# Performance work log

Hardware: AMD Instinct MI355X
Metric: run time of the kernel (lower is better)

The kernel has to match this reference:

```python
import jax, jax.numpy as jnp
import numpy as np

B, N, H, HEADS, F, L = 32, 256, 512, 8, 2048, 8
D = H // HEADS  # per-head dim
EPS = 1e-5


def _layernorm(x, scale, bias):
    mu = jnp.mean(x, axis=-1, keepdims=True)
    var = jnp.mean(jnp.square(x - mu), axis=-1, keepdims=True)
    return (x - mu) * jax.lax.rsqrt(var + EPS) * scale + bias


def setup_inputs() -> dict:
    key = jax.random.key(0)
    ks = jax.random.split(key, 12)
    s = 0.02
    inp = {
        "x": jax.random.normal(ks[0], (B, N, H), jnp.float32),
        "attn_bias": jax.random.normal(ks[1], (B, HEADS, N, N), jnp.float32),
        "ln1_s": jnp.ones((L, H), jnp.float32),
        "ln1_b": jnp.zeros((L, H), jnp.float32),
        "wq": s * jax.random.normal(ks[2], (L, H, H), jnp.float32),
        "bq": jnp.zeros((L, H), jnp.float32),
        "wk": s * jax.random.normal(ks[3], (L, H, H), jnp.float32),
        "bk": jnp.zeros((L, H), jnp.float32),
        "wv": s * jax.random.normal(ks[4], (L, H, H), jnp.float32),
        "bv": jnp.zeros((L, H), jnp.float32),
        "wo": s * jax.random.normal(ks[5], (L, H, H), jnp.float32),
        "bo": jnp.zeros((L, H), jnp.float32),
        "ln2_s": jnp.ones((L, H), jnp.float32),
        "ln2_b": jnp.zeros((L, H), jnp.float32),
        "w1": s * jax.random.normal(ks[6], (L, H, F), jnp.float32),
        "b1": jnp.zeros((L, F), jnp.float32),
        "w2": s * jax.random.normal(ks[7], (L, F, H), jnp.float32),
        "b2": jnp.zeros((L, H), jnp.float32),
    }
    return inp


def reference(x, attn_bias, ln1_s, ln1_b, wq, bq, wk, bk, wv, bv, wo, bo,
              ln2_s, ln2_b, w1, b1, w2, b2):
    scale = D ** (-0.5)
    for l in range(L):
        # --- self attention block ---
        y = _layernorm(x, ln1_s[l], ln1_b[l])
        q = (y @ wq[l] + bq[l]).reshape(B, N, HEADS, D) * scale
        k = (y @ wk[l] + bk[l]).reshape(B, N, HEADS, D)
        v = (y @ wv[l] + bv[l]).reshape(B, N, HEADS, D)
        scores = jnp.einsum("bqhd,bkhd->bhqk", q, k) + attn_bias
        probs = jax.nn.softmax(scores, axis=-1)
        ctx = jnp.einsum("bhqk,bkhd->bqhd", probs, v).reshape(B, N, H)
        x = x + ctx @ wo[l] + bo[l]
        # --- FFN block ---
        y = _layernorm(x, ln2_s[l], ln2_b[l])
        y = jax.nn.gelu(y @ w1[l] + b1[l], approximate=False)
        x = x + y @ w2[l] + b2[l]
    return x
```

## Files before the change

### kernel.cpp

```cpp
#include <hip/hip_runtime.h>
#include <hip/hip_bf16.h>
#include <math.h>

typedef __bf16 bf16;
typedef __bf16 bf16x8 __attribute__((ext_vector_type(8)));
typedef __bf16 bf16x4 __attribute__((ext_vector_type(4)));
typedef float  f32x4  __attribute__((ext_vector_type(4)));

#define DEV __device__ __forceinline__

DEV f32x4 mfma16(bf16x8 a, bf16x8 b, f32x4 c) {
    return __builtin_amdgcn_mfma_f32_16x16x32_bf16(a, b, c, 0, 0, 0);
}

DEV void gload16(const bf16* g, bf16* l) {
    __builtin_amdgcn_global_load_lds(
        (const __attribute__((address_space(1))) void*)g,
        (__attribute__((address_space(3))) void*)l, 16, 0, 0);
}

template <int MODE>
__global__ __launch_bounds__(256, 3) void gemm_k(
    const bf16* __restrict__ A, const bf16* __restrict__ Bt,
    const float* __restrict__ bias, bf16* __restrict__ Cb,
    bf16* __restrict__ vt, int K, int ldC)
{
    __shared__ bf16 As[128 * 32];
    __shared__ bf16 Bs[128 * 32];
    const int tid  = threadIdx.x;
    const int lane = tid & 63;
    const int w    = tid >> 6;
    const int wm   = w & 1, wn = w >> 1;
    const long tm  = (long)blockIdx.y * 128;
    const long tn  = (long)blockIdx.x * 128;

    f32x4 acc[4][4] = {};

    const int r0 = tid >> 2;
    const int cc = ((tid & 3) ^ ((r0 >> 1) & 3)) * 8;
    const bf16* Ag = A  + (tm + r0) * K + cc;
    const bf16* Bg = Bt + (tn + r0) * K + cc;
    const long rstep = (long)64 * K;
    bf16* lA0 = &As[tid * 8];
    bf16* lA1 = &As[(tid + 256) * 8];
    bf16* lB0 = &Bs[tid * 8];
    bf16* lB1 = &Bs[(tid + 256) * 8];

    int am[4], bn[4];
#pragma unroll
    for (int i = 0; i < 4; ++i) {
        int ra = wm * 64 + i * 16 + (lane & 15);
        am[i]  = ra * 32 + (((lane >> 4) ^ ((ra >> 1) & 3)) * 8);
        int rb = wn * 64 + i * 16 + (lane & 15);
        bn[i]  = rb * 32 + (((lane >> 4) ^ ((rb >> 1) & 3)) * 8);
    }

    for (int k0 = 0; k0 < K; k0 += 32) {
        __syncthreads();
        gload16(Ag + k0,         lA0);
        gload16(Ag + rstep + k0, lA1);
        gload16(Bg + k0,         lB0);
        gload16(Bg + rstep + k0, lB1);
        __syncthreads();
        bf16x8 a[4], b[4];
#pragma unroll
        for (int i = 0; i < 4; ++i) a[i] = *(const bf16x8*)&As[am[i]];
#pragma unroll
        for (int i = 0; i < 4; ++i) b[i] = *(const bf16x8*)&Bs[bn[i]];
#pragma unroll
        for (int mi = 0; mi < 4; ++mi)
#pragma unroll
            for (int ni = 0; ni < 4; ++ni)
                acc[mi][ni] = mfma16(a[mi], b[ni], acc[mi][ni]);
    }

#pragma unroll
    for (int mi = 0; mi < 4; ++mi) {
        const long rbase = tm + wm * 64 + mi * 16 + ((lane >> 4) << 2);
#pragma unroll
        for (int ni = 0; ni < 4; ++ni) {
            const long col = tn + wn * 64 + ni * 16 + (lane & 15);
            const float bv = bias[col];
            float v[4];
#pragma unroll
            for (int r = 0; r < 4; ++r) {
                v[r] = acc[mi][ni][r] + bv;
                if constexpr (MODE == 1)
                    v[r] = 0.5f * v[r] * (1.0f + erff(v[r] * 0.70710678118654752f));
            }
            bool toV = false;
            if constexpr (MODE == 2) toV = (col >= 1024);
            if (toV) {
                const int cv = (int)col - 1024;
                const long bh = (rbase >> 8) * 8 + (cv >> 6);
                bf16x4 pk;
#pragma unroll
                for (int r = 0; r < 4; ++r) pk[r] = (bf16)v[r];
                *(bf16x4*)&vt[(bh * 64 + (cv & 63)) * 256 + (rbase & 255)] = pk;
            } else {
#pragma unroll
                for (int r = 0; r < 4; ++r)
                    Cb[(rbase + r) * (long)ldC + col] = (bf16)v[r];
            }
        }
    }
}

__global__ __launch_bounds__(256, 3) void gemm_dk(
    const bf16* __restrict__ A, const bf16* __restrict__ Bt,
    bf16* __restrict__ D, int K, int Ks)
{
    __shared__ bf16 As[128 * 32];
    __shared__ bf16 Bs[128 * 32];
    const int tid  = threadIdx.x;
    const int lane = tid & 63;
    const int w    = tid >> 6;
    const int wm   = w & 1, wn = w >> 1;
    const long tm  = (long)blockIdx.y * 128;
    const long tn  = (long)blockIdx.x * 128;
    const int kbase = blockIdx.z * Ks;

    f32x4 acc[4][4] = {};

    const int r0 = tid >> 2;
    const int cc = ((tid & 3) ^ ((r0 >> 1) & 3)) * 8;
    const bf16* Ag = A  + (tm + r0) * K + kbase + cc;
    const bf16* Bg = Bt + (tn + r0) * K + kbase + cc;
    const long rstep = (long)64 * K;
    bf16* lA0 = &As[tid * 8];
    bf16* lA1 = &As[(tid + 256) * 8];
    bf16* lB0 = &Bs[tid * 8];
    bf16* lB1 = &Bs[(tid + 256) * 8];

    int am[4], bn[4];
#pragma unroll
    for (int i = 0; i < 4; ++i) {
        int ra = wm * 64 + i * 16 + (lane & 15);
        am[i]  = ra * 32 + (((lane >> 4) ^ ((ra >> 1) & 3)) * 8);
        int rb = wn * 64 + i * 16 + (lane & 15);
        bn[i]  = rb * 32 + (((lane >> 4) ^ ((rb >> 1) & 3)) * 8);
    }

    for (int k0 = 0; k0 < Ks; k0 += 32) {
        __syncthreads();
        gload16(Ag + k0,         lA0);
        gload16(Ag + rstep + k0, lA1);
        gload16(Bg + k0,         lB0);
        gload16(Bg + rstep + k0, lB1);
        __syncthreads();
        bf16x8 a[4], b[4];
#pragma unroll
        for (int i = 0; i < 4; ++i) a[i] = *(const bf16x8*)&As[am[i]];
#pragma unroll
        for (int i = 0; i < 4; ++i) b[i] = *(const bf16x8*)&Bs[bn[i]];
#pragma unroll
        for (int mi = 0; mi < 4; ++mi)
#pragma unroll
            for (int ni = 0; ni < 4; ++ni)
                acc[mi][ni] = mfma16(a[mi], b[ni], acc[mi][ni]);
    }

    bf16* Dp = D + (long)blockIdx.z * 8192 * 512;
#pragma unroll
    for (int mi = 0; mi < 4; ++mi) {
        const long rbase = tm + wm * 64 + mi * 16 + ((lane >> 4) << 2);
#pragma unroll
        for (int ni = 0; ni < 4; ++ni) {
            const long col = tn + wn * 64 + ni * 16 + (lane & 15);
#pragma unroll
            for (int r = 0; r < 4; ++r)
                Dp[(rbase + r) * 512 + col] = (bf16)acc[mi][ni][r];
        }
    }
}

__global__ __launch_bounds__(256, 4) void attn_k(
    const bf16* __restrict__ qkv, const bf16* __restrict__ vt,
    const float* __restrict__ bias, bf16* __restrict__ ctx)
{
    __shared__ bf16 smem[256 * 72];
    bf16* Ks = smem;

    const int tid = threadIdx.x, lane = tid & 63, w = tid >> 6;
    const int qt = blockIdx.x & 3;
    const int h  = (blockIdx.x >> 2) & 7;
    const int b  = blockIdx.x >> 5;
    const long qkv_base = (long)b * 256 * 1536;

#pragma unroll
    for (int i = 0; i < 8; ++i) {
        int p = i * 256 + tid;
        int n = p >> 3, kk = (p & 7) * 8;
        uint4 v = *(const uint4*)(qkv + qkv_base + (long)n * 1536 + 512 + h * 64 + kk);
        *(uint4*)&Ks[n * 72 + kk] = v;
    }

    const int qr0 = qt * 64 + w * 16;
    bf16x8 aq0, aq1;
    {
        const bf16* g = qkv + qkv_base + (long)(qr0 + (lane & 15)) * 1536 + h * 64 + ((lane >> 4) * 8);
        aq0 = *(const bf16x8*)g;
        aq1 = *(const bf16x8*)(g + 32);
    }
    __syncthreads();

    f32x4 s[16];
    const float* bb = bias + (((long)(b * 8 + h)) * 256 + qr0) * 256;
#pragma unroll
    for (int ct = 0; ct < 16; ++ct) {
        const int col = ct * 16 + (lane & 15);
        f32x4 c;
#pragma unroll
        for (int r = 0; r < 4; ++r)
            c[r] = bb[(long)((lane >> 4) * 4 + r) * 256 + col];
        bf16x8 k0 = *(const bf16x8*)&Ks[(ct * 16 + (lane & 15)) * 72 + ((lane >> 4) * 8)];
        bf16x8 k1 = *(const bf16x8*)&Ks[(ct * 16 + (lane & 15)) * 72 + 32 + ((lane >> 4) * 8)];
        c = mfma16(aq0, k0, c);
        c = mfma16(aq1, k1, c);
        s[ct] = c;
    }

    float m[4] = {-1e30f, -1e30f, -1e30f, -1e30f};
#pragma unroll
    for (int ct = 0; ct < 16; ++ct)
#pragma unroll
        for (int r = 0; r < 4; ++r) m[r] = fmaxf(m[r], s[ct][r]);
#pragma unroll
    for (int r = 0; r < 4; ++r)
#pragma unroll
        for (int off = 1; off < 16; off <<= 1)
            m[r] = fmaxf(m[r], __shfl_xor(m[r], off));
    float l[4] = {0.f, 0.f, 0.f, 0.f};
#pragma unroll
    for (int ct = 0; ct < 16; ++ct)
#pragma unroll
        for (int r = 0; r < 4; ++r) {
            float p = __expf(s[ct][r] - m[r]);
            s[ct][r] = p;
            l[r] += p;
        }
#pragma unroll
    for (int r = 0; r < 4; ++r) {
#pragma unroll
        for (int off = 1; off < 16; off <<= 1) l[r] += __shfl_xor(l[r], off);
        l[r] = 1.0f / l[r];
    }

    __syncthreads();
    bf16* P = smem + w * (16 * 264);
#pragma unroll
    for (int ct = 0; ct < 16; ++ct)
#pragma unroll
        for (int r = 0; r < 4; ++r)
            P[(long)((lane >> 4) * 4 + r) * 264 + ct * 16 + (lane & 15)] = (bf16)s[ct][r];

    bf16x8 ap[8];
#pragma unroll
    for (int nk = 0; nk < 8; ++nk)
        ap[nk] = *(const bf16x8*)&P[(lane & 15) * 264 + nk * 32 + (lane >> 4) * 8];

    const bf16* vg = vt + (long)(b * 8 + h) * 64 * 256;
    f32x4 o[4];
#pragma unroll
    for (int dt = 0; dt < 4; ++dt) {
        f32x4 c = {};
#pragma unroll
        for (int nk = 0; nk < 8; ++nk) {
            bf16x8 bv = *(const bf16x8*)&vg[(dt * 16 + (lane & 15)) * 256 + nk * 32 + (lane >> 4) * 8];
            c = mfma16(ap[nk], bv, c);
        }
        o[dt] = c;
    }

#pragma unroll
    for (int dt = 0; dt < 4; ++dt) {
        const int col = h * 64 + dt * 16 + (lane & 15);
#pragma unroll
        for (int r = 0; r < 4; ++r) {
            const long row = (long)b * 256 + qr0 + (lane >> 4) * 4 + r;
            ctx[row * 512 + col] = (bf16)(o[dt][r] * l[r]);
        }
    }
}

template <int NS>
__global__ __launch_bounds__(256) void ln_k(
    const float* __restrict__ x, float* __restrict__ xout,
    const bf16* __restrict__ d, const float* __restrict__ rbias,
    const float* __restrict__ sc, const float* __restrict__ bi,
    bf16* __restrict__ y)
{
    const int lane = threadIdx.x & 63;
    const long row = (long)blockIdx.x * 4 + (threadIdx.x >> 6);
    const float* xr = x + row * 512;
    float v[8];
    *(float4*)&v[0] = ((const float4*)xr)[lane * 2];
    *(float4*)&v[4] = ((const float4*)xr)[lane * 2 + 1];
    if constexpr (NS == 2) {
        bf16x8 d0 = *(const bf16x8*)&d[row * 512 + lane * 8];
        bf16x8 d1 = *(const bf16x8*)&d[(long)8192 * 512 + row * 512 + lane * 8];
        float b4[8];
        *(float4*)&b4[0] = ((const float4*)rbias)[lane * 2];
        *(float4*)&b4[4] = ((const float4*)rbias)[lane * 2 + 1];
#pragma unroll
        for (int j = 0; j < 8; ++j)
            v[j] += (float)d0[j] + (float)d1[j] + b4[j];
        float* xo = xout + row * 512;
        ((float4*)xo)[lane * 2]     = *(const float4*)&v[0];
        ((float4*)xo)[lane * 2 + 1] = *(const float4*)&v[4];
    }
    float sum = 0.f;
#pragma unroll
    for (int j = 0; j < 8; ++j) sum += v[j];
#pragma unroll
    for (int off = 1; off < 64; off <<= 1) sum += __shfl_xor(sum, off);
    const float mu = sum * (1.0f / 512.0f);
    float sq = 0.f;
#pragma unroll
    for (int j = 0; j < 8; ++j) { float dd = v[j] - mu; sq += dd * dd; }
#pragma unroll
    for (int off = 1; off < 64; off <<= 1) sq += __shfl_xor(sq, off);
    const float rs = rsqrtf(sq * (1.0f / 512.0f) + 1e-5f);
    bf16* yr = y + row * 512;
#pragma unroll
    for (int j = 0; j < 8; ++j) {
        int c = lane * 8 + j;
        yr[c] = (bf16)((v[j] - mu) * rs * sc[c] + bi[c]);
    }
}

__global__ __launch_bounds__(256) void addout_k(
    const float* __restrict__ x, const bf16* __restrict__ d,
    const float* __restrict__ rbias, float* __restrict__ out)
{
    const int lane = threadIdx.x & 63;
    const long row = (long)blockIdx.x * 4 + (threadIdx.x >> 6);
    float v[8];
    *(float4*)&v[0] = ((const float4*)(x + row * 512))[lane * 2];
    *(float4*)&v[4] = ((const float4*)(x + row * 512))[lane * 2 + 1];
    bf16x8 d0 = *(const bf16x8*)&d[row * 512 + lane * 8];
    bf16x8 d1 = *(const bf16x8*)&d[(long)8192 * 512 + row * 512 + lane * 8];
    float b4[8];
    *(float4*)&b4[0] = ((const float4*)rbias)[lane * 2];
    *(float4*)&b4[4] = ((const float4*)rbias)[lane * 2 + 1];
#pragma unroll
    for (int j = 0; j < 8; ++j)
        v[j] += (float)d0[j] + (float)d1[j] + b4[j];
    float* o = out + row * 512;
    ((float4*)o)[lane * 2]     = *(const float4*)&v[0];
    ((float4*)o)[lane * 2 + 1] = *(const float4*)&v[4];
}

__global__ __launch_bounds__(256) void transpose_k(
    const float* __restrict__ wq, const float* __restrict__ wk,
    const float* __restrict__ wv, const float* __restrict__ wo,
    const float* __restrict__ w1, const float* __restrict__ w2,
    bf16* __restrict__ qkvT, bf16* __restrict__ woT,
    bf16* __restrict__ w1T, bf16* __restrict__ w2T)
{
    __shared__ float tile[32][33];
    const int tid = threadIdx.x, tx = tid & 31, ty = tid >> 5;
    const int l = blockIdx.x / 3072;
    const int r = blockIdx.x % 3072;

    const float* In = nullptr;
    bf16* Out = nullptr;
    int Nd, tk, tn, rowOff = 0, ldO;
    float scale = 1.0f;
    if (r < 1024) {
        const int which = r >> 8, t = r & 255;
        tn = t >> 4; tk = t & 15; Nd = 512; ldO = 512;
        const long woff = (long)l * 512 * 512;
        if (which == 0)      { In = wq + woff; Out = qkvT + (long)l * 1536 * 512; rowOff = 0;    scale = 0.125f; }
        else if (which == 1) { In = wk + woff; Out = qkvT + (long)l * 1536 * 512; rowOff = 512;  }
        else if (which == 2) { In = wv + woff; Out = qkvT + (long)l * 1536 * 512; rowOff = 1024; }
        else                 { In = wo + woff; Out = woT + woff; }
    } else if (r < 2048) {
        const int t = r - 1024;
        tn = t >> 4; tk = t & 15; Nd = 2048; ldO = 512;
        In = w1 + (long)l * 512 * 2048; Out = w1T + (long)l * 2048 * 512;
    } else {
        const int t = r - 2048;
        tn = t & 15; tk = t >> 4; Nd = 512; ldO = 2048;
        In = w2 + (long)l * 2048 * 512; Out = w2T + (long)l * 512 * 2048;
    }
    const int gk = tk * 32, gn = tn * 32;
#pragma unroll
    for (int j = 0; j < 4; ++j) {
        int rr = ty + j * 8;
        tile[rr][tx] = In[(long)(gk + rr) * Nd + gn + tx] * scale;
    }
    __syncthreads();
#pragma unroll
    for (int j = 0; j < 4; ++j) {
        int rr = ty + j * 8;
        Out[(long)(rowOff + gn + rr) * ldO + gk + tx] = (bf16)tile[tx][rr];
    }
}

__global__ void biasq_k(const float* __restrict__ bq, const float* __restrict__ bk,
                        const float* __restrict__ bv, float* __restrict__ bqkv)
{
    int i = blockIdx.x * 256 + threadIdx.x;
    if (i >= 8 * 1536) return;
    int l = i / 1536, j = i % 1536;
    float v;
    if (j < 512)       v = bq[l * 512 + j] * 0.125f;
    else if (j < 1024) v = bk[l * 512 + j - 512];
    else               v = bv[l * 512 + j - 1024];
    bqkv[i] = v;
}

extern "C" void kernel_launch(void* const* d_in, const int* in_sizes, int n_in,
                              void* d_out, int out_size, void* d_ws, size_t ws_size,
                              hipStream_t stream)
{
    (void)in_sizes; (void)n_in; (void)out_size; (void)ws_size;
    const float* x    = (const float*)d_in[0];
    const float* ab   = (const float*)d_in[1];
    const float* ln1s = (const float*)d_in[2];
    const float* ln1b = (const float*)d_in[3];
    const float* wq   = (const float*)d_in[4];
    const float* bq   = (const float*)d_in[5];
    const float* wk   = (const float*)d_in[6];
    const float* bk   = (const float*)d_in[7];
    const float* wv   = (const float*)d_in[8];
    const float* bv   = (const float*)d_in[9];
    const float* wo   = (const float*)d_in[10];
    const float* bo   = (const float*)d_in[11];
    const float* ln2s = (const float*)d_in[12];
    const float* ln2b = (const float*)d_in[13];
    const float* w1   = (const float*)d_in[14];
    const float* b1   = (const float*)d_in[15];
    const float* w2   = (const float*)d_in[16];
    const float* b2   = (const float*)d_in[17];

    char* ws = (char*)d_ws;
    float* xf   = (float*)ws;
    bf16* y     = (bf16*)(ws + 16777216);
    bf16* ctx   = y;
    bf16* qkv   = (bf16*)(ws + 16777216 + 8388608);
    bf16* ffn   = qkv;
    bf16* vt    = qkv + (long)8192 * 1536;
    bf16* dbuf  = (bf16*)(ws + 16777216 + 8388608 + 33554432);
    bf16* wqkvT = dbuf + (long)2 * 8192 * 512;
    bf16* woT   = wqkvT + (long)8 * 1536 * 512;
    bf16* w1T   = woT + (long)8 * 512 * 512;
    bf16* w2T   = w1T + (long)8 * 2048 * 512;
    float* bqkv = (float*)(w2T + (long)8 * 512 * 2048);

    hipMemcpyAsync(xf, x, (size_t)8192 * 512 * 4, hipMemcpyDeviceToDevice, stream);
    transpose_k<<<24576, 256, 0, stream>>>(wq, wk, wv, wo, w1, w2, wqkvT, woT, w1T, w2T);
    biasq_k<<<48, 256, 0, stream>>>(bq, bk, bv, bqkv);

    for (int l = 0; l < 8; ++l) {
        if (l == 0)
            ln_k<0><<<2048, 256, 0, stream>>>(xf, nullptr, nullptr, nullptr,
                                              ln1s, ln1b, y);
        else
            ln_k<2><<<2048, 256, 0, stream>>>(xf, xf, dbuf, b2 + (l - 1) * 512,
                                              ln1s + l * 512, ln1b + l * 512, y);
        gemm_k<2><<<dim3(12, 64), 256, 0, stream>>>(
            y, wqkvT + (long)l * 1536 * 512, bqkv + l * 1536, qkv, vt, 512, 1536);
        attn_k<<<1024, 256, 0, stream>>>(qkv, vt, ab, ctx);
        gemm_dk<<<dim3(4, 64, 2), 256, 0, stream>>>(
            ctx, woT + (long)l * 512 * 512, dbuf, 512, 256);
        ln_k<2><<<2048, 256, 0, stream>>>(xf, xf, dbuf, bo + l * 512,
                                          ln2s + l * 512, ln2b + l * 512, y);
        gemm_k<1><<<dim3(16, 64), 256, 0, stream>>>(
            y, w1T + (long)l * 2048 * 512, b1 + l * 2048, ffn, nullptr, 512, 2048);
        gemm_dk<<<dim3(4, 64, 2), 256, 0, stream>>>(
            ffn, w2T + (long)l * 512 * 2048, dbuf, 2048, 1024);
    }
    addout_k<<<2048, 256, 0, stream>>>(xf, dbuf, b2 + 7 * 512, (float*)d_out);
}
```

Baseline: 1.388 ms.

## Double-buffer GEMM LDS tiles, stage V-transpose via LDS, use polynomial GELU

Both GEMM kernels now keep two LDS buffers, so the global-to-LDS load of the next K-slice is issued while MFMAs run on the current one, and one barrier is removed per step. The QKV GEMM's V-transpose epilogue is staged through shared memory so it writes 16-byte coalesced rows instead of scattered 8-byte stores. The GELU epilogue swaps erff for an Abramowitz-Stegun polynomial with __expf, which slightly changes numerical accuracy. LDS use doubles per block, which may lower occupancy below the launch-bounds target.

```diff
diff --git a/kernel.cpp b/kernel.cpp
--- a/kernel.cpp
+++ b/kernel.cpp
@@ -17,6 +17,17 @@
     __builtin_amdgcn_global_load_lds(
         (const __attribute__((address_space(1))) void*)g,
         (__attribute__((address_space(3))) void*)l, 16, 0, 0);
+}
+
+DEV float gelu_f(float v) {
+    float xs = v * 0.70710678118654752f;
+    float ax = fabsf(xs);
+    float t  = 1.0f / (1.0f + 0.3275911f * ax);
+    float p  = t * (0.254829592f + t * (-0.284496736f + t * (1.421413741f +
+               t * (-1.453152027f + t * 1.061405429f))));
+    float er = 1.0f - p * __expf(-ax * ax);
+    er = copysignf(er, xs);
+    return 0.5f * v * (1.0f + er);
 }
 
 template <int MODE>
@@ -25,8 +36,10 @@
     const float* __restrict__ bias, bf16* __restrict__ Cb,
     bf16* __restrict__ vt, int K, int ldC)
 {
-    __shared__ bf16 As[128 * 32];
-    __shared__ bf16 Bs[128 * 32];
+    __shared__ bf16 smem[(MODE == 2) ? 17408 : 16384];
+    bf16* As = smem;
+    bf16* Bs = smem + 8192;
+
     const int tid  = threadIdx.x;
     const int lane = tid & 63;
     const int w    = tid >> 6;
@@ -41,10 +54,6 @@
     const bf16* Ag = A  + (tm + r0) * K + cc;
     const bf16* Bg = Bt + (tn + r0) * K + cc;
     const long rstep = (long)64 * K;
-    bf16* lA0 = &As[tid * 8];
-    bf16* lA1 = &As[(tid + 256) * 8];
-    bf16* lB0 = &Bs[tid * 8];
-    bf16* lB1 = &Bs[(tid + 256) * 8];
 
     int am[4], bn[4];
 #pragma unroll
@@ -55,23 +64,71 @@
         bn[i]  = rb * 32 + (((lane >> 4) ^ ((rb >> 1) & 3)) * 8);
     }
 
-    for (int k0 = 0; k0 < K; k0 += 32) {
+#define STAGE(buf, kk)                                        \
+    do {                                                      \
+        gload16(Ag + (kk),         &As[(buf)*4096 + tid*8]);  \
+        gload16(Ag + rstep + (kk), &As[(buf)*4096 + 2048 + tid*8]); \
+        gload16(Bg + (kk),         &Bs[(buf)*4096 + tid*8]);  \
+        gload16(Bg + rstep + (kk), &Bs[(buf)*4096 + 2048 + tid*8]); \
+    } while (0)
+
+#define COMPUTE(buf)                                                    \
+    do {                                                                \
+        bf16x8 a[4], b[4];                                              \
+        _Pragma("unroll")                                               \
+        for (int i = 0; i < 4; ++i) a[i] = *(const bf16x8*)&As[(buf)*4096 + am[i]]; \
+        _Pragma("unroll")                                               \
+        for (int i = 0; i < 4; ++i) b[i] = *(const bf16x8*)&Bs[(buf)*4096 + bn[i]]; \
+        _Pragma("unroll")                                               \
+        for (int mi = 0; mi < 4; ++mi)                                  \
+            _Pragma("unroll")                                           \
+            for (int ni = 0; ni < 4; ++ni)                              \
+                acc[mi][ni] = mfma16(a[mi], b[ni], acc[mi][ni]);        \
+    } while (0)
+
+    STAGE(0, 0);
+    __syncthreads();
+    for (int k0 = 0; k0 < K; k0 += 64) {
+        STAGE(1, k0 + 32);
+        COMPUTE(0);
         __syncthreads();
-        gload16(Ag + k0,         lA0);
-        gload16(Ag + rstep + k0, lA1);
-        gload16(Bg + k0,         lB0);
-        gload16(Bg + rstep + k0, lB1);
+        if (k0 + 64 < K) STAGE(0, k0 + 64);
+        COMPUTE(1);
         __syncthreads();
-        bf16x8 a[4], b[4];
-#pragma unroll
-        for (int i = 0; i < 4; ++i) a[i] = *(const bf16x8*)&As[am[i]];
-#pragma unroll
-        for (int i = 0; i < 4; ++i) b[i] = *(const bf16x8*)&Bs[bn[i]];
-#pragma unroll
-        for (int mi = 0; mi < 4; ++mi)
-#pragma unroll
-            for (int ni = 0; ni < 4; ++ni)
-                acc[mi][ni] = mfma16(a[mi], b[ni], acc[mi][ni]);
+    }
+
+    bool vpath = false;
+    if constexpr (MODE == 2) vpath = (tn >= 1024);
+
+    if (vpath) {
+        bf16* Ct = smem;
+#pragma unroll
+        for (int mi = 0; mi < 4; ++mi) {
+            const int rowL = wm * 64 + mi * 16 + ((lane >> 4) << 2);
+#pragma unroll
+            for (int ni = 0; ni < 4; ++ni) {
+                const int colL = wn * 64 + ni * 16 + (lane & 15);
+                const float bv = bias[tn + colL];
+                bf16x4 pk;
+#pragma unroll
+                for (int r = 0; r < 4; ++r) pk[r] = (bf16)(acc[mi][ni][r] + bv);
+                *(bf16x4*)&Ct[colL * 136 + rowL] = pk;
+            }
+        }
+        __syncthreads();
+        const int b_blk = (int)(tm >> 8);
+        const int nin   = (int)(tm & 255);
+        const int cvb   = (int)(tn - 1024);
+#pragma unroll
+        for (int j = 0; j < 8; ++j) {
+            int idx = j * 256 + tid;
+            int c   = idx >> 4;
+            int nc  = (idx & 15) * 8;
+            bf16x8 vv = *(const bf16x8*)&Ct[c * 136 + nc];
+            int cv = cvb + c;
+            *(bf16x8*)&vt[(((long)b_blk * 8 + (cv >> 6)) * 64 + (cv & 63)) * 256 + nin + nc] = vv;
+        }
+        return;
     }
 
 #pragma unroll
@@ -81,37 +138,26 @@
         for (int ni = 0; ni < 4; ++ni) {
             const long col = tn + wn * 64 + ni * 16 + (lane & 15);
             const float bv = bias[col];
-            float v[4];
 #pragma unroll
             for (int r = 0; r < 4; ++r) {
-                v[r] = acc[mi][ni][r] + bv;
-                if constexpr (MODE == 1)
-                    v[r] = 0.5f * v[r] * (1.0f + erff(v[r] * 0.70710678118654752f));
+                float v = acc[mi][ni][r] + bv;
+                if constexpr (MODE == 1) v = gelu_f(v);
+                Cb[(rbase + r) * (long)ldC + col] = (bf16)v;
             }
-            bool toV = false;
-            if constexpr (MODE == 2) toV = (col >= 1024);
-            if (toV) {
-                const int cv = (int)col - 1024;
-                const long bh = (rbase >> 8) * 8 + (cv >> 6);
-                bf16x4 pk;
-#pragma unroll
-                for (int r = 0; r < 4; ++r) pk[r] = (bf16)v[r];
-                *(bf16x4*)&vt[(bh * 64 + (cv & 63)) * 256 + (rbase & 255)] = pk;
-            } else {
-#pragma unroll
-                for (int r = 0; r < 4; ++r)
-                    Cb[(rbase + r) * (long)ldC + col] = (bf16)v[r];
-            }
-        }
-    }
+        }
+    }
+#undef STAGE
+#undef COMPUTE
 }
 
 __global__ __launch_bounds__(256, 3) void gemm_dk(
     const bf16* __restrict__ A, const bf16* __restrict__ Bt,
     bf16* __restrict__ D, int K, int Ks)
 {
-    __shared__ bf16 As[128 * 32];
-    __shared__ bf16 Bs[128 * 32];
+    __shared__ bf16 smem[16384];
+    bf16* As = smem;
+    bf16* Bs = smem + 8192;
+
     const int tid  = threadIdx.x;
     const int lane = tid & 63;
     const int w    = tid >> 6;
@@ -127,10 +173,6 @@
     const bf16* Ag = A  + (tm + r0) * K + kbase + cc;
     const bf16* Bg = Bt + (tn + r0) * K + kbase + cc;
     const long rstep = (long)64 * K;
-    bf16* lA0 = &As[tid * 8];
-    bf16* lA1 = &As[(tid + 256) * 8];
-    bf16* lB0 = &Bs[tid * 8];
-    bf16* lB1 = &Bs[(tid + 256) * 8];
 
     int am[4], bn[4];
 #pragma unroll
@@ -141,23 +183,37 @@
         bn[i]  = rb * 32 + (((lane >> 4) ^ ((rb >> 1) & 3)) * 8);
     }
 
-    for (int k0 = 0; k0 < Ks; k0 += 32) {
+#define STAGE(buf, kk)                                        \
+    do {                                                      \
+        gload16(Ag + (kk),         &As[(buf)*4096 + tid*8]);  \
+        gload16(Ag + rstep + (kk), &As[(buf)*4096 + 2048 + tid*8]); \
+        gload16(Bg + (kk),         &Bs[(buf)*4096 + tid*8]);  \
+        gload16(Bg + rstep + (kk), &Bs[(buf)*4096 + 2048 + tid*8]); \
+    } while (0)
+
+#define COMPUTE(buf)                                                    \
+    do {                                                                \
+        bf16x8 a[4], b[4];                                              \
+        _Pragma("unroll")                                               \
+        for (int i = 0; i < 4; ++i) a[i] = *(const bf16x8*)&As[(buf)*4096 + am[i]]; \
+        _Pragma("unroll")                                               \
+        for (int i = 0; i < 4; ++i) b[i] = *(const bf16x8*)&Bs[(buf)*4096 + bn[i]]; \
+        _Pragma("unroll")                                               \
+        for (int mi = 0; mi < 4; ++mi)                                  \
+            _Pragma("unroll")                                           \
+            for (int ni = 0; ni < 4; ++ni)                              \
+                acc[mi][ni] = mfma16(a[mi], b[ni], acc[mi][ni]);        \
+    } while (0)
+
+    STAGE(0, 0);
+    __syncthreads();
+    for (int k0 = 0; k0 < Ks; k0 += 64) {
+        STAGE(1, k0 + 32);
+        COMPUTE(0);
         __syncthreads();
-        gload16(Ag + k0,         lA0);
-        gload16(Ag + rstep + k0, lA1);
-        gload16(Bg + k0,         lB0);
-        gload16(Bg + rstep + k0, lB1);
+        if (k0 + 64 < Ks) STAGE(0, k0 + 64);
+        COMPUTE(1);
         __syncthreads();
-        bf16x8 a[4], b[4];
-#pragma unroll
-        for (int i = 0; i < 4; ++i) a[i] = *(const bf16x8*)&As[am[i]];
-#pragma unroll
-        for (int i = 0; i < 4; ++i) b[i] = *(const bf16x8*)&Bs[bn[i]];
-#pragma unroll
-        for (int mi = 0; mi < 4; ++mi)
-#pragma unroll
-            for (int ni = 0; ni < 4; ++ni)
-                acc[mi][ni] = mfma16(a[mi], b[ni], acc[mi][ni]);
     }
 
     bf16* Dp = D + (long)blockIdx.z * 8192 * 512;
@@ -172,6 +228,8 @@
                 Dp[(rbase + r) * 512 + col] = (bf16)acc[mi][ni][r];
         }
     }
+#undef STAGE
+#undef COMPUTE
 }
 
 __global__ __launch_bounds__(256, 4) void attn_k(
```

Measured after the change: 1.358 ms. -2.1%, faster.
